# Kernel tuning notes

Measured on AMD Instinct MI355X. Metric: run time of the kernel, lower is better.

Reference implementation:

```python
import jax, jax.numpy as jnp
import numpy as np

# Supernet configuration (matches init_kwargs)
HIDDEN = [1024, 2048]
HEADS = [8, 16]
ABITS = [4, 8]
WBITS = [4, 8]
B, S = 4, 4096
MAX_IN = max(HIDDEN)            # 2048
MAX_OUT = max(HIDDEN)           # min(heads)*max(hidden)//min(heads) = 2048


def fake_quant(v, s, bit):
    """LSQ-style symmetric fake quantization with straight-through rounding."""
    qp = float(2 ** (bit - 1) - 1)
    qn = -float(2 ** (bit - 1))
    vs = jnp.clip(v / s, qn, qp)
    vq = vs + jax.lax.stop_gradient(jnp.round(vs) - vs)  # STE round
    return vq * s


def setup_inputs() -> dict:
    key = jax.random.key(0)
    k1, k2, k3, k4 = jax.random.split(key, 4)
    x = jax.random.normal(k1, (B, S, MAX_IN), jnp.float32)
    weights = jax.random.uniform(k2, (16,), jnp.float32)  # arch mixing coeffs
    W = jax.random.normal(k3, (MAX_OUT, MAX_IN), jnp.float32) * 0.02
    b = jax.random.normal(k4, (MAX_OUT,), jnp.float32) * 0.02
    # init_weight_scale: LSQ init 2*mean(|W|)/sqrt(Qp) per weight bitwidth
    w_scales = jnp.stack([2.0 * jnp.mean(jnp.abs(W)) / jnp.sqrt(float(2 ** (bit - 1) - 1))
                          for bit in WBITS])
    a_scales = jnp.ones((len(ABITS),), jnp.float32)
    return {"x": x, "weights": weights, "W": W, "b": b,
            "a_scales": a_scales, "w_scales": w_scales}


def reference(x, weights, W, b, a_scales, w_scales):
    # Non-argmax mixture path (reverse=False):
    # for each (hidden_i, heads_j, abit_m, wbit_n): slice W to
    # [out_dim, in_dim], zero-pad to [MAX_OUT, MAX_IN] (== masking, since
    # per-tensor fake-quant maps 0 -> 0), quantize, and weighted-accumulate.
    # Quantized x / W depend only on abit / wbit, so compute each once.
    qx = [fake_quant(x, a_scales[m], ABITS[m]) for m in range(len(ABITS))]   # [B,S,MAX_IN]
    qw = [fake_quant(W, w_scales[n], WBITS[n]) for n in range(len(WBITS))]  # [MAX_OUT,MAX_IN]
    out_idx = jnp.arange(MAX_OUT)
    in_idx = jnp.arange(MAX_IN)

    w_mix = jnp.zeros_like(W)
    x_mix = jnp.zeros_like(x)
    b_mix = jnp.zeros_like(b)
    k = 0
    for i, h in enumerate(HIDDEN):
        for j, nh in enumerate(HEADS):
            head_dim = h // nh
            out_dim = nh * head_dim  # == h when divisible
            in_dim = h
            wmask = (out_idx[:, None] < out_dim) & (in_idx[None, :] < in_dim)
            bmask = out_idx < out_dim
            for m in range(len(ABITS)):
                for n in range(len(WBITS)):
                    a = weights[k]
                    w_mix = w_mix + a * jnp.where(wmask, qw[n], 0.0)
                    x_mix = x_mix + a * qx[m]
                    b_mix = b_mix + a * jnp.where(bmask, b, 0.0)
                    k += 1
    # out = F.linear(x_mix, w_mix, b_mix)
    out = jnp.einsum('bsi,oi->bso', x_mix, w_mix) + b_mix
    return out
```

## Files before the change

### kernel.cpp

```cpp
#include <hip/hip_runtime.h>
#include <hip/hip_bf16.h>
#include <stdint.h>

#define MDIM 16384
#define NDIM 2048
#define KDIM 2048

typedef __attribute__((ext_vector_type(4))) float f32x4;
typedef __attribute__((ext_vector_type(8))) short s16x8;

__device__ __forceinline__ void gload_lds16(const __hip_bfloat16* g, void* l) {
    __builtin_amdgcn_global_load_lds(
        (const __attribute__((address_space(1))) void*)g,
        (__attribute__((address_space(3))) void*)l,
        16, 0, 0);
}


__global__ __launch_bounds__(256) void prep_x(
    const float* __restrict__ x, const float* __restrict__ weights,
    const float* __restrict__ a_scales, __hip_bfloat16* __restrict__ xq)
{
    float A0 = 0.f, A1 = 0.f;
    #pragma unroll
    for (int k = 0; k < 16; ++k) {
        float w = weights[k];
        if (((k >> 1) & 1) == 0) A0 += w; else A1 += w;
    }
    const float s0 = a_scales[0], s1 = a_scales[1];
    const float r0 = 1.f / s0, r1 = 1.f / s1;

    size_t idx = ((size_t)blockIdx.x * 256 + threadIdx.x) * 8;
    const f32x4* xv = (const f32x4*)(x + idx);
    f32x4 v0 = xv[0], v1 = xv[1];
    float vals[8] = {v0.x, v0.y, v0.z, v0.w, v1.x, v1.y, v1.z, v1.w};

    union { s16x8 v; __hip_bfloat16 h[8]; } u;
    #pragma unroll
    for (int j = 0; j < 8; ++j) {
        float q0 = rintf(fminf(fmaxf(vals[j] * r0, -8.f),   7.f)) * s0;
        float q1 = rintf(fminf(fmaxf(vals[j] * r1, -128.f), 127.f)) * s1;
        u.h[j] = __float2bfloat16(A0 * q0 + A1 * q1);
    }
    *(s16x8*)(xq + idx) = u.v;
}

__global__ __launch_bounds__(256) void prep_w(
    const float* __restrict__ W, const float* __restrict__ weights,
    const float* __restrict__ w_scales, __hip_bfloat16* __restrict__ wq)
{
    float c00 = weights[0] + weights[2]  + weights[4]  + weights[6];
    float c01 = weights[1] + weights[3]  + weights[5]  + weights[7];
    float c10 = weights[8] + weights[10] + weights[12] + weights[14];
    float c11 = weights[9] + weights[11] + weights[13] + weights[15];

    const float s0 = w_scales[0], s1 = w_scales[1];
    const float r0 = 1.f / s0, r1 = 1.f / s1;

    size_t idx = ((size_t)blockIdx.x * 256 + threadIdx.x) * 8;
    const int o = (int)(idx >> 11);
    const int c = (int)(idx & 2047);
    const bool inner = (o < 1024) && (c < 1024);
    const float k0 = inner ? (c00 + c10) : c10;
    const float k1 = inner ? (c01 + c11) : c11;

    const f32x4* wv = (const f32x4*)(W + idx);
    f32x4 v0 = wv[0], v1 = wv[1];
    float vals[8] = {v0.x, v0.y, v0.z, v0.w, v1.x, v1.y, v1.z, v1.w};

    union { s16x8 v; __hip_bfloat16 h[8]; } u;
    #pragma unroll
    for (int j = 0; j < 8; ++j) {
        float q0 = rintf(fminf(fmaxf(vals[j] * r0, -8.f),   7.f)) * s0;
        float q1 = rintf(fminf(fmaxf(vals[j] * r1, -128.f), 127.f)) * s1;
        u.h[j] = __float2bfloat16(k0 * q0 + k1 * q1);
    }
    *(s16x8*)(wq + idx) = u.v;
}

__global__ __launch_bounds__(256) void prep_b(
    const float* __restrict__ b, const float* __restrict__ weights,
    float* __restrict__ bm)
{
    int o = blockIdx.x * 256 + threadIdx.x;
    if (o >= NDIM) return;
    float S1 = 0.f, S0 = 0.f;
    #pragma unroll
    for (int k = 0; k < 8; ++k)  S0 += weights[k];
    #pragma unroll
    for (int k = 8; k < 16; ++k) S1 += weights[k];
    bm[o] = b[o] * ((o < 1024) ? (S0 + S1) : S1);
}


#define BM 256
#define BN 256
#define NCH 64
#define ASLOT 16384
#define BREG  65536

#define MFMA(a, b, c) __builtin_amdgcn_mfma_f32_16x16x32_bf16((a), (b), (c), 0, 0, 0)

#define CHUNK(S, T)                                                          \
  {                                                                          \
    asm volatile("" ::: "memory");      \
    s16x8 af[8], bf[4];                                                      \
    _Pragma("unroll")                                                        \
    for (int m_ = 0; m_ < 8; ++m_)                                           \
      af[m_] = *(const s16x8*)(lds + (S) * ASLOT + aoff + m_ * 1024);        \
    _Pragma("unroll")                                                        \
    for (int n_ = 0; n_ < 4; ++n_)                                           \
      bf[n_] = *(const s16x8*)(lds + BREG + (S) * ASLOT + boff + n_ * 1024); \
    gload_lds16(As0 + kg * 32, lds + (T) * ASLOT + ldoff);                   \
    gload_lds16(As1 + kg * 32, lds + (T) * ASLOT + 8192 + ldoff);            \
    gload_lds16(Bs0 + kg * 32, lds + BREG + (T) * ASLOT + ldoff);            \
    gload_lds16(Bs1 + kg * 32, lds + BREG + (T) * ASLOT + 8192 + ldoff);     \
    kg = (kg + 1) & (NCH - 1);                                               \
    __builtin_amdgcn_s_setprio(1);                                           \
    _Pragma("unroll")                                                        \
    for (int m_ = 0; m_ < 8; ++m_) {                                         \
      acc[m_][0] = MFMA(af[m_], bf[0], acc[m_][0]);                          \
      acc[m_][1] = MFMA(af[m_], bf[1], acc[m_][1]);                          \
      acc[m_][2] = MFMA(af[m_], bf[2], acc[m_][2]);                          \
      acc[m_][3] = MFMA(af[m_], bf[3], acc[m_][3]);                          \
    }                                                                        \
    __builtin_amdgcn_s_setprio(0);                                           \
    asm volatile("s_waitcnt vmcnt(8)" ::: "memory");   \
    __builtin_amdgcn_s_barrier();                                            \
  }

__global__ __launch_bounds__(512, 2) void gemm256(
    const __hip_bfloat16* __restrict__ A,
    const __hip_bfloat16* __restrict__ B,
    const float* __restrict__ bias,
    float* __restrict__ C)
{
    __shared__ char lds[8 * ASLOT];

    const int tid  = threadIdx.x;
    const int lane = tid & 63;
    const int wid  = tid >> 6;
    const int wm   = wid >> 2;
    const int wn   = wid & 3;

    const int bid  = blockIdx.x;
    const int swz  = (bid & 7) * 64 + (bid >> 3);
    const int brow = (swz >> 3) * BM;
    const int bcol = (swz & 7) * BN;

    const int csw = (tid & 3) ^ ((tid >> 3) & 3);
    const __hip_bfloat16* As0 = A + (size_t)(brow + (tid >> 2)) * KDIM + csw * 8;
    const __hip_bfloat16* As1 = As0 + (size_t)128 * KDIM;
    const __hip_bfloat16* Bs0 = B + (size_t)(bcol + (tid >> 2)) * KDIM + csw * 8;
    const __hip_bfloat16* Bs1 = Bs0 + (size_t)128 * KDIM;
    const int ldoff = tid * 16;

    const int fr  = lane & 15;
    const int l16 = lane >> 4;
    const int xr  = (l16 ^ ((fr >> 1) & 3)) * 16;
    const int aoff = (wm * 128 + fr) * 64 + xr;
    const int boff = (wn * 64  + fr) * 64 + xr;

    f32x4 acc[8][4];
    #pragma unroll
    for (int m = 0; m < 8; ++m)
        #pragma unroll
        for (int n = 0; n < 4; ++n)
            acc[m][n] = (f32x4){0.f, 0.f, 0.f, 0.f};

    int kg = 3;

    #pragma unroll
    for (int q = 0; q < 3; ++q) {
        gload_lds16(As0 + q * 32, lds + q * ASLOT + ldoff);
        gload_lds16(As1 + q * 32, lds + q * ASLOT + 8192 + ldoff);
        gload_lds16(Bs0 + q * 32, lds + BREG + q * ASLOT + ldoff);
        gload_lds16(Bs1 + q * 32, lds + BREG + q * ASLOT + 8192 + ldoff);
    }
    asm volatile("s_waitcnt vmcnt(8)" ::: "memory");
    __builtin_amdgcn_s_barrier();

    #pragma unroll 1
    for (int it = 0; it < NCH / 4; ++it) {
        CHUNK(0, 3);
        CHUNK(1, 0);
        CHUNK(2, 1);
        CHUNK(3, 2);
    }
    asm volatile("s_waitcnt vmcnt(0) lgkmcnt(0)" ::: "memory");

    const int ccol0 = bcol + wn * 64 + fr;
    const int crow0 = brow + wm * 128 + l16 * 4;
    float bv[4];
    #pragma unroll
    for (int n = 0; n < 4; ++n) bv[n] = bias[ccol0 + n * 16];

    #pragma unroll
    for (int m = 0; m < 8; ++m) {
        #pragma unroll
        for (int j = 0; j < 4; ++j) {
            float* Crow = C + (size_t)(crow0 + m * 16 + j) * NDIM;
            #pragma unroll
            for (int n = 0; n < 4; ++n)
                Crow[ccol0 + n * 16] = acc[m][n][j] + bv[n];
        }
    }
}


extern "C" void kernel_launch(void* const* d_in, const int* in_sizes, int n_in,
                              void* d_out, int out_size, void* d_ws, size_t ws_size,
                              hipStream_t stream) {
    const float* x        = (const float*)d_in[0];
    const float* weights  = (const float*)d_in[1];
    const float* W        = (const float*)d_in[2];
    const float* b        = (const float*)d_in[3];
    const float* a_scales = (const float*)d_in[4];
    const float* w_scales = (const float*)d_in[5];
    float* out = (float*)d_out;

    __hip_bfloat16* xq = (__hip_bfloat16*)d_ws;
    __hip_bfloat16* wq = (__hip_bfloat16*)((char*)d_ws + 67108864);
    float*          bm = (float*)((char*)d_ws + 67108864 + 8388608);

    prep_w<<<dim3((NDIM * KDIM) / (256 * 8)), dim3(256), 0, stream>>>(W, weights, w_scales, wq);
    prep_b<<<dim3(NDIM / 256), dim3(256), 0, stream>>>(b, weights, bm);
    prep_x<<<dim3(((size_t)MDIM * KDIM) / (256 * 8)), dim3(256), 0, stream>>>(x, weights, a_scales, xq);
    gemm256<<<dim3((MDIM / BM) * (NDIM / BN)), dim3(512), 0, stream>>>(xq, wq, bm, out);
}
```

Measured before the change: 162.5 us.

## Restructure GEMM mainloop into double-buffered K=64 tiles with four interleaved phases

Replaces the four-slot K=32 ring buffer with a two-slot double buffer of K=64 tiles. Each tile is processed in four phases that split the M dimension and the K halves. Each phase reads half of the A fragments, reuses the B fragments across M halves, and stages one quarter of the next tile's global-to-LDS loads. The aim is finer-grained overlap of LDS reads, global prefetch and MFMA work, plus fewer fragment registers live at once. In exchange it adds barriers per K step and cuts the prefetch depth to a single tile ahead, which may expose memory latency.

Result: no change. 163.8 us (+0.8%).

```diff
diff --git a/kernel.cpp b/kernel.cpp
--- a/kernel.cpp
+++ b/kernel.cpp
@@ -93,41 +93,52 @@
 }
 
 
-#define BM 256
-#define BN 256
-#define NCH 64
-#define ASLOT 16384
-#define BREG  65536
+#define NT 32
+#define REGION 16384
+#define SLOTB  65536
 
 #define MFMA(a, b, c) __builtin_amdgcn_mfma_f32_16x16x32_bf16((a), (b), (c), 0, 0, 0)
 
-#define CHUNK(S, T)                                                          \
+#define PHASE(SL, MH, KH, RD_BF, STG_B, STG_KH, DO_VM)                       \
   {                                                                          \
-    asm volatile("" ::: "memory");      \
-    s16x8 af[8], bf[4];                                                      \
+    const char* pa_ = lds + (SL) * SLOTB + (KH) * REGION;                    \
     _Pragma("unroll")                                                        \
-    for (int m_ = 0; m_ < 8; ++m_)                                           \
-      af[m_] = *(const s16x8*)(lds + (S) * ASLOT + aoff + m_ * 1024);        \
-    _Pragma("unroll")                                                        \
-    for (int n_ = 0; n_ < 4; ++n_)                                           \
-      bf[n_] = *(const s16x8*)(lds + BREG + (S) * ASLOT + boff + n_ * 1024); \
-    gload_lds16(As0 + kg * 32, lds + (T) * ASLOT + ldoff);                   \
-    gload_lds16(As1 + kg * 32, lds + (T) * ASLOT + 8192 + ldoff);            \
-    gload_lds16(Bs0 + kg * 32, lds + BREG + (T) * ASLOT + ldoff);            \
-    gload_lds16(Bs1 + kg * 32, lds + BREG + (T) * ASLOT + 8192 + ldoff);     \
-    kg = (kg + 1) & (NCH - 1);                                               \
+    for (int i_ = 0; i_ < 4; ++i_)                                           \
+      af[i_] = *(const s16x8*)(pa_ + (MH) * 4096 + i_ * 1024 + aoff);        \
+    if (RD_BF) {                                                             \
+      const char* pb_ = lds + (SL) * SLOTB + (2 + (KH)) * REGION;            \
+      _Pragma("unroll")                                                      \
+      for (int n_ = 0; n_ < 4; ++n_)                                         \
+        bf[n_] = *(const s16x8*)(pb_ + n_ * 1024 + boff);                    \
+    }                                                                        \
+    {                                                                        \
+      char* d_ = lds + ((SL) ^ 1) * SLOTB                                    \
+               + ((STG_B) ? (2 + (STG_KH)) : (STG_KH)) * REGION + ldoff;     \
+      const __hip_bfloat16* s_ = ((STG_B) ? Bs : As) + kg * 64 + (STG_KH) * 32; \
+      gload_lds16(s_, d_);                                                   \
+      gload_lds16(s_ + (size_t)128 * KDIM, d_ + 8192);                       \
+    }                                                                        \
+    if (DO_VM) asm volatile("s_waitcnt vmcnt(4)" ::: "memory");              \
+    __builtin_amdgcn_s_barrier();                                            \
+    asm volatile("s_waitcnt lgkmcnt(0)" ::: "memory");                       \
     __builtin_amdgcn_s_setprio(1);                                           \
     _Pragma("unroll")                                                        \
-    for (int m_ = 0; m_ < 8; ++m_) {                                         \
-      acc[m_][0] = MFMA(af[m_], bf[0], acc[m_][0]);                          \
-      acc[m_][1] = MFMA(af[m_], bf[1], acc[m_][1]);                          \
-      acc[m_][2] = MFMA(af[m_], bf[2], acc[m_][2]);                          \
-      acc[m_][3] = MFMA(af[m_], bf[3], acc[m_][3]);                          \
+    for (int i_ = 0; i_ < 4; ++i_) {                                         \
+      acc[(MH)*4+i_][0] = MFMA(af[i_], bf[0], acc[(MH)*4+i_][0]);            \
+      acc[(MH)*4+i_][1] = MFMA(af[i_], bf[1], acc[(MH)*4+i_][1]);            \
+      acc[(MH)*4+i_][2] = MFMA(af[i_], bf[2], acc[(MH)*4+i_][2]);            \
+      acc[(MH)*4+i_][3] = MFMA(af[i_], bf[3], acc[(MH)*4+i_][3]);            \
     }                                                                        \
     __builtin_amdgcn_s_setprio(0);                                           \
-    asm volatile("s_waitcnt vmcnt(8)" ::: "memory");   \
     __builtin_amdgcn_s_barrier();                                            \
   }
+
+#define KTILE(SL)                                                            \
+    PHASE(SL, 0, 0, 1, 0, 0, 0);    \
+    PHASE(SL, 1, 0, 0, 1, 0, 1);         \
+    PHASE(SL, 0, 1, 1, 0, 1, 0);    \
+    PHASE(SL, 1, 1, 0, 1, 1, 1);         \
+    kg = (kg + 1) & (NT - 1);
 
 __global__ __launch_bounds__(512, 2) void gemm256(
     const __hip_bfloat16* __restrict__ A,
@@ -135,7 +146,7 @@
     const float* __restrict__ bias,
     float* __restrict__ C)
 {
-    __shared__ char lds[8 * ASLOT];
+    __shared__ char lds[2 * SLOTB];
 
     const int tid  = threadIdx.x;
     const int lane = tid & 63;
@@ -145,21 +156,19 @@
 
     const int bid  = blockIdx.x;
     const int swz  = (bid & 7) * 64 + (bid >> 3);
-    const int brow = (swz >> 3) * BM;
-    const int bcol = (swz & 7) * BN;
+    const int brow = (swz >> 3) * 256;
+    const int bcol = (swz & 7) * 256;
 
     const int csw = (tid & 3) ^ ((tid >> 3) & 3);
-    const __hip_bfloat16* As0 = A + (size_t)(brow + (tid >> 2)) * KDIM + csw * 8;
-    const __hip_bfloat16* As1 = As0 + (size_t)128 * KDIM;
-    const __hip_bfloat16* Bs0 = B + (size_t)(bcol + (tid >> 2)) * KDIM + csw * 8;
-    const __hip_bfloat16* Bs1 = Bs0 + (size_t)128 * KDIM;
+    const __hip_bfloat16* As = A + (size_t)(brow + (tid >> 2)) * KDIM + csw * 8;
+    const __hip_bfloat16* Bs = B + (size_t)(bcol + (tid >> 2)) * KDIM + csw * 8;
     const int ldoff = tid * 16;
 
     const int fr  = lane & 15;
     const int l16 = lane >> 4;
     const int xr  = (l16 ^ ((fr >> 1) & 3)) * 16;
-    const int aoff = (wm * 128 + fr) * 64 + xr;
-    const int boff = (wn * 64  + fr) * 64 + xr;
+    const int aoff = wm * 8192 + fr * 64 + xr;
+    const int boff = wn * 4096 + fr * 64 + xr;
 
     f32x4 acc[8][4];
     #pragma unroll
@@ -168,24 +177,27 @@
         for (int n = 0; n < 4; ++n)
             acc[m][n] = (f32x4){0.f, 0.f, 0.f, 0.f};
 
-    int kg = 3;
-
-    #pragma unroll
-    for (int q = 0; q < 3; ++q) {
-        gload_lds16(As0 + q * 32, lds + q * ASLOT + ldoff);
-        gload_lds16(As1 + q * 32, lds + q * ASLOT + 8192 + ldoff);
-        gload_lds16(Bs0 + q * 32, lds + BREG + q * ASLOT + ldoff);
-        gload_lds16(Bs1 + q * 32, lds + BREG + q * ASLOT + 8192 + ldoff);
-    }
-    asm volatile("s_waitcnt vmcnt(8)" ::: "memory");
+    s16x8 af[4], bf[4];
+    int kg = 1;
+
+    {
+        #pragma unroll
+        for (int h = 0; h < 4; ++h) {
+            const int  kh = h >> 1;
+            const int  isB = h & 1;
+            char* d = lds + (isB ? (2 + kh) : kh) * REGION + ldoff;
+            const __hip_bfloat16* s = (isB ? Bs : As) + kh * 32;
+            gload_lds16(s, d);
+            gload_lds16(s + (size_t)128 * KDIM, d + 8192);
+        }
+    }
+    asm volatile("s_waitcnt vmcnt(4)" ::: "memory");
     __builtin_amdgcn_s_barrier();
 
     #pragma unroll 1
-    for (int it = 0; it < NCH / 4; ++it) {
-        CHUNK(0, 3);
-        CHUNK(1, 0);
-        CHUNK(2, 1);
-        CHUNK(3, 2);
+    for (int it = 0; it < NT / 2; ++it) {
+        KTILE(0);
+        KTILE(1);
     }
     asm volatile("s_waitcnt vmcnt(0) lgkmcnt(0)" ::: "memory");
 
@@ -226,5 +238,5 @@
     prep_w<<<dim3((NDIM * KDIM) / (256 * 8)), dim3(256), 0, stream>>>(W, weights, w_scales, wq);
     prep_b<<<dim3(NDIM / 256), dim3(256), 0, stream>>>(b, weights, bm);
     prep_x<<<dim3(((size_t)MDIM * KDIM) / (256 * 8)), dim3(256), 0, stream>>>(x, weights, a_scales, xq);
-    gemm256<<<dim3((MDIM / BM) * (NDIM / BN)), dim3(512), 0, stream>>>(xq, wq, bm, out);
-}
+    gemm256<<<dim3((MDIM / 256) * (NDIM / 256)), dim3(512), 0, stream>>>(xq, wq, bm, out);
+}
```
